# Kernel optimization log

Hardware: AMD Instinct MI355X
Metric: run time of the kernel (lower is better)

## Reference

```python
import jax, jax.numpy as jnp
import numpy as np

D_MODEL = 256
D_INNER = 512    # expand=2
D_STATE = 16
D_CONV = 4
DT_RANK = 16     # ceil(256/16)
N_BLOCKS = 4
EPS = 1e-5


def setup_inputs() -> dict:
    key = jax.random.key(0)
    ks = jax.random.split(key, 8)
    s = 0.02
    return {
        "x": jax.random.normal(ks[0], (1, 4, D_MODEL, 32, 32), jnp.float32),
        "norm_w": jnp.ones((N_BLOCKS, D_MODEL), jnp.float32),
        "norm_b": jnp.zeros((N_BLOCKS, D_MODEL), jnp.float32),
        "in_w": jax.random.normal(ks[1], (N_BLOCKS, 2 * D_INNER, D_MODEL), jnp.float32) * s,
        "conv_w": jax.random.normal(ks[2], (N_BLOCKS, D_INNER, D_CONV), jnp.float32) * s,
        "conv_b": jnp.zeros((N_BLOCKS, D_INNER), jnp.float32),
        "xproj_w": jax.random.normal(ks[3], (N_BLOCKS, DT_RANK + 2 * D_STATE, D_INNER), jnp.float32) * s,
        "dtproj_w": jax.random.normal(ks[4], (N_BLOCKS, D_INNER, DT_RANK), jnp.float32) * s,
        "dtproj_b": jax.random.normal(ks[5], (N_BLOCKS, D_INNER), jnp.float32) * s,
        "A_log": jnp.tile(jnp.log(jnp.arange(1, D_STATE + 1, dtype=jnp.float32))[None, None, :],
                          (N_BLOCKS, D_INNER, 1)),
        "Dp": jnp.ones((N_BLOCKS, D_INNER), jnp.float32),
        "out_w": jax.random.normal(ks[6], (N_BLOCKS, D_MODEL, D_INNER), jnp.float32) * s,
    }


def _layernorm(x, w, b):
    mu = jnp.mean(x, axis=-1, keepdims=True)
    var = jnp.var(x, axis=-1, keepdims=True)
    return (x - mu) / jnp.sqrt(var + EPS) * w + b


def _mamba(h, in_w, conv_w, conv_b, xproj_w, dtproj_w, dtproj_b, A_log, Dp, out_w):
    # h: (B, L, d_model)
    B, L, _ = h.shape
    xz = h @ in_w.T                                   # (B, L, 2*d_inner)
    x, z = jnp.split(xz, 2, axis=-1)
    # causal depthwise conv1d, kernel size D_CONV
    xp = jnp.pad(x, ((0, 0), (D_CONV - 1, 0), (0, 0)))
    xc = sum(xp[:, k:k + L, :] * conv_w[:, k] for k in range(D_CONV)) + conv_b
    x = jax.nn.silu(xc)                               # (B, L, d_inner)
    dbl = x @ xproj_w.T                               # (B, L, dt_rank + 2*d_state)
    dt = dbl[..., :DT_RANK]
    Bm = dbl[..., DT_RANK:DT_RANK + D_STATE]          # (B, L, n)
    Cm = dbl[..., DT_RANK + D_STATE:]                 # (B, L, n)
    dt = jax.nn.softplus(dt @ dtproj_w.T + dtproj_b)  # (B, L, d_inner)
    A = -jnp.exp(A_log)                               # (d_inner, n)
    dA = jnp.exp(dt[..., None] * A)                   # (B, L, d_inner, n)
    dBx = dt[..., None] * Bm[:, :, None, :] * x[..., None]

    def step(hprev, inp):
        dA_t, dBx_t, C_t = inp
        hcur = dA_t * hprev + dBx_t                   # (B, d_inner, n)
        return hcur, jnp.einsum('bdn,bn->bd', hcur, C_t)

    h0 = jnp.zeros((B, D_INNER, D_STATE), x.dtype)
    _, y = jax.lax.scan(step, h0, (dA.transpose(1, 0, 2, 3),
                                   dBx.transpose(1, 0, 2, 3),
                                   Cm.transpose(1, 0, 2)))
    y = y.transpose(1, 0, 2)                          # (B, L, d_inner)
    y = (y + Dp * x) * jax.nn.silu(z)
    return y @ out_w.T                                # (B, L, d_model)


def _forward(x, norm_w, norm_b, in_w, conv_w, conv_b, xproj_w, dtproj_w, dtproj_b, A_log, Dp, out_w):
    b, n, c, h, w = x.shape
    hs = x.reshape(b * n, c, h * w).transpose(0, 2, 1)  # (bn, hw, c)

    def blk(i, hidden, resid):
        resid = hidden if resid is None else resid + hidden
        hn = _layernorm(resid, norm_w[i], norm_b[i])
        out = _mamba(hn, in_w[i], conv_w[i], conv_b[i], xproj_w[i],
                     dtproj_w[i], dtproj_b[i], A_log[i], Dp[i], out_w[i])
        return out, resid

    res = None
    for i in range(2):  # pairs of (forward, backward-flipped) blocks
        hf, rf = blk(2 * i, hs, res)
        hb, rb = blk(2 * i + 1, hs[:, ::-1], None if res is None else res[:, ::-1])
        hs = hf + hb[:, ::-1]
        res = rf + rb[:, ::-1]
    res = res + hs
    return res.transpose(0, 2, 1).reshape(b, n, c, h, w)


def reference(x, norm_w, norm_b, in_w, conv_w, conv_b, xproj_w, dtproj_w, dtproj_b, A_log, Dp, out_w):
    return _forward(x, norm_w, norm_b, in_w, conv_w, conv_b, xproj_w,
                    dtproj_w, dtproj_b, A_log, Dp, out_w)
```

## Files before the change

kernel.cpp:

```cpp
#include <hip/hip_runtime.h>
#include <math.h>


__device__ __forceinline__ float sigmoidf_(float x){ return 1.f/(1.f+__expf(-x)); }
__device__ __forceinline__ short bf16_(float x){
  unsigned u = __float_as_uint(x);
  u += 0x7FFFu + ((u>>16)&1u);
  return (short)(u>>16);
}
__device__ __forceinline__ float f32_(short s){
  return __uint_as_float(((unsigned)(unsigned short)s)<<16);
}

using fragAB = __attribute__((ext_vector_type(8))) short;
using fragC  = __attribute__((ext_vector_type(4))) float;

__global__ __launch_bounds__(256) void k_transpose_in(const float* __restrict__ x, float* __restrict__ hs){
  __shared__ float tile[32][33];
  int b = blockIdx.z;
  int l0 = blockIdx.x*32, c0 = blockIdx.y*32;
  int tx = threadIdx.x, ty = threadIdx.y;
  #pragma unroll
  for (int j=0;j<32;j+=8)
    tile[ty+j][tx] = x[(size_t)b*262144 + (size_t)(c0+ty+j)*1024 + l0 + tx];
  __syncthreads();
  #pragma unroll
  for (int j=0;j<32;j+=8)
    hs[(size_t)b*262144 + (size_t)(l0+ty+j)*256 + (c0+tx)] = tile[tx][ty+j];
}

__global__ __launch_bounds__(256) void k_final(const float* __restrict__ racc, const float* __restrict__ hs, float* __restrict__ out){
  __shared__ float tile[32][33];
  int b = blockIdx.z;
  int l0 = blockIdx.x*32, c0 = blockIdx.y*32;
  int tx = threadIdx.x, ty = threadIdx.y;
  #pragma unroll
  for (int j=0;j<32;j+=8){
    size_t idx = (size_t)b*262144 + (size_t)(l0+ty+j)*256 + c0+tx;
    tile[ty+j][tx] = 2.f*racc[idx] + hs[idx];
  }
  __syncthreads();
  #pragma unroll
  for (int j=0;j<32;j+=8)
    out[(size_t)b*262144 + (size_t)(c0+ty+j)*1024 + l0+tx] = tile[tx][ty+j];
}

__global__ __launch_bounds__(256) void k_ln(const float* __restrict__ hs, float* __restrict__ racc, short* __restrict__ hn_f,
  const float* __restrict__ nw, const float* __restrict__ nb, int layer0, int first){
  int row = blockIdx.x, c = threadIdx.x;
  size_t idx = (size_t)row*256 + c;
  float r = hs[idx];
  if (!first) r += 2.f*racc[idx];
  racc[idx] = r;
  float s1=r, s2=r*r;
  #pragma unroll
  for (int o=32;o>=1;o>>=1){ s1+=__shfl_xor(s1,o); s2+=__shfl_xor(s2,o); }
  __shared__ float red[8];
  int wid=c>>6, lane=c&63;
  if (lane==0){ red[wid]=s1; red[4+wid]=s2; }
  __syncthreads();
  s1 = red[0]+red[1]+red[2]+red[3];
  s2 = red[4]+red[5]+red[6]+red[7];
  float mu = s1*(1.f/256.f);
  float var = s2*(1.f/256.f) - mu*mu;
  float inv = rsqrtf(var + 1e-5f);
  float nv = (r-mu)*inv;
  size_t fo = (((size_t)(row>>4)*32 + (c>>3))*16 + (row&15))*8 + (c&7);
  hn_f[fo]           = bf16_(nv*nw[layer0*256+c] + nb[layer0*256+c]);
  hn_f[1048576 + fo] = bf16_(nv*nw[(layer0+1)*256+c] + nb[(layer0+1)*256+c]);
}

__global__ __launch_bounds__(256) void k_wconv(
  const float* __restrict__ inw, const float* __restrict__ xpw,
  const float* __restrict__ dtw, const float* __restrict__ otw,
  short* __restrict__ f_inw, short* __restrict__ f_xpw,
  short* __restrict__ f_dtw, short* __restrict__ f_otw)
{
  int b = blockIdx.x, tid = threadIdx.x;
  int which, layer, idx;
  if (b < 4096){ which=0; layer=b>>10; idx=((b&1023)<<8)+tid; }
  else if (b < 4480){ int r=b-4096; which=1; layer=r/96;  idx=(r%96)*256+tid; }
  else if (b < 4736){ int r=b-4480; which=2; layer=r>>6;  idx=(r&63)*256+tid; }
  else              { int r=b-4736; which=3; layer=r>>9;  idx=(r&511)*256+tid; }
  const float* src; short* dst; int R,K,Kp;
  if (which==0){ src=inw; dst=f_inw; R=1024; K=256; Kp=256; }
  else if (which==1){ src=xpw; dst=f_xpw; R=48; K=512; Kp=512; }
  else if (which==2){ src=dtw; dst=f_dtw; R=512; K=16; Kp=32; }
  else { src=otw; dst=f_otw; R=256; K=512; Kp=512; }
  int per = (R>>4)*(Kp>>3)*128;
  int e = idx & 127, tile = idx >> 7;
  int nkt = Kp>>3;
  int kt = tile % nkt, rt = tile / nkt;
  int r = rt*16 + (e>>3), k = kt*8 + (e&7);
  float v = (k<K) ? src[((size_t)layer*R + r)*K + k] : 0.f;
  dst[(size_t)layer*per + idx] = bf16_(v);
}

__global__ __launch_bounds__(256) void k_mm4(
  const short* __restrict__ Af, long sA,
  const short* __restrict__ Wf, long sW,
  const short* __restrict__ A2f, const short* __restrict__ W2f,
  float* __restrict__ Cb, long sC,
  int K, int ldc, int mode,
  short* __restrict__ aux1, long sAux1,
  short* __restrict__ aux2, long sAux2)
{
  int z = blockIdx.z;
  int tid = threadIdx.x;
  int lane = tid & 63, wid = tid >> 6;
  int wm = wid & 1, wn = wid >> 1;
  int K8 = K >> 3;
  int mt_base = blockIdx.y*8 + wm*4;
  int nt_base = blockIdx.x*8 + wn*4;
  const int loff = lane*8;
  fragC acc[4][4] = {};
  const short* Aps[2] = { Af + (size_t)z*sA, A2f };
  const short* Wps[2] = { Wf + (size_t)z*sW, W2f };
  int nseg = A2f ? 2 : 1;
  for (int sgi=0; sgi<nseg; ++sgi){
    const short* A = Aps[sgi];
    const short* W = Wps[sgi];
    for (int kt=0; kt<K8; kt+=4){
      fragAB a[4], b[4];
      #pragma unroll
      for (int i=0;i<4;++i)
        a[i] = *(const fragAB*)(A + ((size_t)(mt_base+i)*K8 + kt)*128 + loff);
      #pragma unroll
      for (int j=0;j<4;++j)
        b[j] = *(const fragAB*)(W + ((size_t)(nt_base+j)*K8 + kt)*128 + loff);
      #pragma unroll
      for (int i=0;i<4;++i)
        #pragma unroll
        for (int j=0;j<4;++j)
          acc[i][j] = __builtin_amdgcn_mfma_f32_16x16x32_bf16(a[i], b[j], acc[i][j], 0,0,0);
    }
  }
  float* C = Cb ? Cb + (size_t)z*sC : nullptr;
  int r0 = (lane>>4)*4;
  int cc = lane & 15;
  #pragma unroll
  for (int i=0;i<4;++i){
    int row = (mt_base+i)*16 + r0;
    #pragma unroll
    for (int j=0;j<4;++j){
      int col = (nt_base+j)*16 + cc;
      #pragma unroll
      for (int r=0;r<4;++r){
        float v = acc[i][j][r];
        int rr = row + r;
        if (mode==3){
          if (col < 512) aux1[(size_t)z*sAux1 + (size_t)rr*512 + col] = bf16_(v);
          else           aux2[(size_t)z*sAux2 + (size_t)rr*512 + (col-512)] = bf16_(v);
        } else {
          C[(size_t)rr*ldc + col] = v;
        }
      }
    }
  }
}

__global__ __launch_bounds__(256) void k_xpdt(
  const short* __restrict__ xc_f, const short* __restrict__ wxp,
  const short* __restrict__ wdt, const float* __restrict__ dtb,
  float* __restrict__ dbl, float* __restrict__ dtv, int layer0)
{
  __shared__ short dt_lds[32][24];
  int z = blockIdx.y;
  int by = blockIdx.x;
  int layer = layer0 + z;
  int tid = threadIdx.x, lane = tid & 63, wn = tid >> 6;
  const short* A = xc_f + (size_t)z*2097152;
  const short* W = wxp + (size_t)layer*24576;
  int mt0 = by*2;
  const int loff = lane*8;
  int r0 = (lane>>4)*4, cc = lane & 15;
  {
    fragC acc[2] = {};
    int nt = wn < 3 ? wn : 2;
    for (int kt=0; kt<64; kt+=4){
      fragAB a0 = *(const fragAB*)(A + ((size_t)(mt0+0)*64 + kt)*128 + loff);
      fragAB a1 = *(const fragAB*)(A + ((size_t)(mt0+1)*64 + kt)*128 + loff);
      fragAB b  = *(const fragAB*)(W + ((size_t)nt*64 + kt)*128 + loff);
      acc[0] = __builtin_amdgcn_mfma_f32_16x16x32_bf16(a0, b, acc[0], 0,0,0);
      acc[1] = __builtin_amdgcn_mfma_f32_16x16x32_bf16(a1, b, acc[1], 0,0,0);
    }
    int col = nt*16 + cc;
    #pragma unroll
    for (int i=0;i<2;++i){
      int lr = i*16 + r0;
      int grow = by*32 + lr;
      #pragma unroll
      for (int r=0;r<4;++r){
        float v = acc[i][r];
        if (wn==1 || wn==2)
          dbl[(size_t)z*196608 + (size_t)(grow+r)*48 + col] = v;
        if (wn==0)
          dt_lds[lr+r][cc] = bf16_(v);
      }
    }
  }
  __syncthreads();
  {
    float* dto = dtv + (size_t)z*2097152;
    const float* bias = dtb + (size_t)layer*512;
    const short* WD = wdt + (size_t)layer*16384;
    int kq = lane >> 4;
    fragAB a2[2];
    #pragma unroll
    for (int i=0;i<2;++i){
      fragAB t = {};
      if (kq < 2){
        #pragma unroll
        for (int j=0;j<8;++j) t[j] = dt_lds[i*16 + (lane&15)][kq*8 + j];
      }
      a2[i] = t;
    }
    #pragma unroll
    for (int c2=0;c2<2;++c2){
      fragC acc2[2][4] = {};
      fragAB b2[4];
      #pragma unroll
      for (int j=0;j<4;++j){
        int ntj = wn*8 + c2*4 + j;
        b2[j] = *(const fragAB*)(WD + ((size_t)ntj*4)*128 + loff);
      }
      #pragma unroll
      for (int i=0;i<2;++i)
        #pragma unroll
        for (int j=0;j<4;++j)
          acc2[i][j] = __builtin_amdgcn_mfma_f32_16x16x32_bf16(a2[i], b2[j], acc2[i][j], 0,0,0);
      #pragma unroll
      for (int i=0;i<2;++i){
        int grow = by*32 + i*16 + r0;
        #pragma unroll
        for (int j=0;j<4;++j){
          int col2 = (wn*8 + c2*4 + j)*16 + cc;
          #pragma unroll
          for (int r=0;r<4;++r){
            float v = acc2[i][j][r] + bias[col2];
            v = (v > 20.f) ? v : log1pf(__expf(v));
            dto[(size_t)(grow+r)*512 + col2] = v;
          }
        }
      }
    }
  }
}

__global__ __launch_bounds__(256) void k_conv(const short* __restrict__ xb, short* __restrict__ xc_f,
  const float* __restrict__ cw, const float* __restrict__ cb, int layer0){
  int idx = blockIdx.x*256 + threadIdx.x;
  int d = idx & 511;
  int t = (idx >> 9) & 1023;
  int sb = idx >> 19;
  int s = sb >> 2, b = sb & 3;
  int layer = layer0 + s;
  const float* w = cw + ((size_t)layer*512 + d)*4;
  float accv = cb[(size_t)layer*512 + d];
  const short* xp = xb + (size_t)s*2097152 + (size_t)b*1024*512 + d;
  if (s==0){
    #pragma unroll
    for (int k=0;k<4;++k){ int tt = t + k - 3; if (tt>=0) accv = fmaf(f32_(xp[(size_t)tt*512]), w[k], accv); }
  } else {
    #pragma unroll
    for (int k=0;k<4;++k){ int tt = t + 3 - k; if (tt<1024) accv = fmaf(f32_(xp[(size_t)tt*512]), w[k], accv); }
  }
  float v = accv * sigmoidf_(accv);
  int row = b*1024 + t;
  xc_f[(size_t)s*2097152 + (((size_t)(row>>4)*64 + (d>>3))*16 + (row&15))*8 + (d&7)] = bf16_(v);
}

#define NCHUNK 64
#define CSTEPS 16

__device__ __forceinline__ float ld_xc(const short* xcf, int row, int d){
  return f32_(xcf[(((size_t)(row>>4)*64 + (d>>3))*16 + (row&15))*8 + (d&7)]);
}

__global__ __launch_bounds__(256) void k_scan_a(
  const float* __restrict__ dtv, const short* __restrict__ xc_f,
  const float* __restrict__ dbl, const float* __restrict__ A_log,
  float* __restrict__ dtsum, float* __restrict__ hF, int layer0)
{
  int d = blockIdx.x*256 + threadIdx.x;
  int k = blockIdx.y;
  int sb = blockIdx.z;
  int s = sb >> 2, b = sb & 3;
  int layer = layer0 + s;
  float Av[16];
  #pragma unroll
  for (int n=0;n<16;++n) Av[n] = -__expf(A_log[((size_t)layer*512 + d)*16 + n]);
  const float* dt_p = dtv + (size_t)sb*524288 + d;
  const short* xcf = xc_f + (size_t)s*2097152;
  const float* bc_p = dbl + (size_t)sb*49152;
  float h[16];
  #pragma unroll
  for (int n=0;n<16;++n) h[n] = 0.f;
  float ssum = 0.f;
  int u0 = k*CSTEPS;
  #pragma unroll
  for (int i=0;i<CSTEPS;++i){
    int u = u0 + i;
    int t = s ? (1023 - u) : u;
    int row = b*1024 + t;
    float dtval = dt_p[(size_t)t*512];
    float xv = ld_xc(xcf, row, d);
    const float4* bp = (const float4*)(bc_p + (size_t)t*48 + 16);
    float4 B0 = bp[0], B1 = bp[1], B2 = bp[2], B3 = bp[3];
    float Bv[16] = {B0.x,B0.y,B0.z,B0.w,B1.x,B1.y,B1.z,B1.w,
                    B2.x,B2.y,B2.z,B2.w,B3.x,B3.y,B3.z,B3.w};
    float w = dtval * xv;
    ssum += dtval;
    #pragma unroll
    for (int n=0;n<16;++n)
      h[n] = fmaf(__expf(dtval*Av[n]), h[n], w*Bv[n]);
  }
  size_t base = (size_t)(sb*NCHUNK + k)*512 + d;
  dtsum[base] = ssum;
  float4* hp = (float4*)(hF + base*16);
  #pragma unroll
  for (int q=0;q<4;++q) hp[q] = make_float4(h[4*q],h[4*q+1],h[4*q+2],h[4*q+3]);
}

__global__ __launch_bounds__(256) void k_scan_c(
  const float* __restrict__ dtsum, float* __restrict__ hF,
  const float* __restrict__ A_log, int layer0)
{
  __shared__ float tile[64][17];
  __shared__ float ds[64];
  int d = blockIdx.x, sb = blockIdx.y;
  int tid = threadIdx.x, lane = tid & 63, w = tid >> 6;
  int layer = layer0 + (sb >> 2);
  size_t base = (size_t)sb*64*8192 + (size_t)d*16;
  {
    int k = tid >> 2, n0 = (tid & 3)*4;
    float4 v = *(const float4*)(hF + base + (size_t)k*8192 + n0);
    tile[k][n0+0]=v.x; tile[k][n0+1]=v.y; tile[k][n0+2]=v.z; tile[k][n0+3]=v.w;
  }
  if (tid < 64) ds[tid] = dtsum[((size_t)sb*64 + tid)*512 + d];
  __syncthreads();
  float dsk = ds[lane];
  #pragma unroll
  for (int p=0;p<4;++p){
    int n = p*4 + w;
    float Av = -__expf(A_log[((size_t)layer*512 + d)*16 + n]);
    float a = __expf(Av * dsk);
    float h = tile[lane][n];
    #pragma unroll
    for (int o=1;o<64;o<<=1){
      float au = __shfl_up(a, o);
      float hu = __shfl_up(h, o);
      if (lane >= o){ h = fmaf(a, hu, h); a *= au; }
    }
    float h0 = __shfl_up(h, 1);
    if (lane == 0) h0 = 0.f;
    tile[lane][n] = h0;
  }
  __syncthreads();
  {
    int k = tid >> 2, n0 = (tid & 3)*4;
    float4 v = make_float4(tile[k][n0], tile[k][n0+1], tile[k][n0+2], tile[k][n0+3]);
    *(float4*)(hF + base + (size_t)k*8192 + n0) = v;
  }
}

__global__ __launch_bounds__(256) void k_scan_b(
  const float* __restrict__ dtv, const short* __restrict__ xc_f, const short* __restrict__ zb,
  const float* __restrict__ dbl, const float* __restrict__ A_log, const float* __restrict__ Dp,
  const float* __restrict__ h0p, short* __restrict__ y_f, int layer0)
{
  int d = blockIdx.x*256 + threadIdx.x;
  int k = blockIdx.y;
  int sb = blockIdx.z;
  int s = sb >> 2, b = sb & 3;
  int layer = layer0 + s;
  float Av[16];
  #pragma unroll
  for (int n=0;n<16;++n) Av[n] = -__expf(A_log[((size_t)layer*512 + d)*16 + n]);
  float Dv = Dp[(size_t)layer*512 + d];
  const float* dt_p = dtv + (size_t)sb*524288 + d;
  const short* xcf = xc_f + (size_t)s*2097152;
  const short* z_p = zb + (size_t)s*2097152 + (size_t)b*1024*512 + d;
  const float* bc_p = dbl + (size_t)sb*49152;
  size_t base = (size_t)(sb*NCHUNK + k)*512 + d;
  float h[16];
  const float4* hp = (const float4*)(h0p + base*16);
  #pragma unroll
  for (int q=0;q<4;++q){
    float4 v = hp[q];
    h[4*q]=v.x; h[4*q+1]=v.y; h[4*q+2]=v.z; h[4*q+3]=v.w;
  }
  short* yo = y_f + (size_t)s*2097152;
  int u0 = k*CSTEPS;
  #pragma unroll
  for (int i=0;i<CSTEPS;++i){
    int u = u0 + i;
    int t = s ? (1023 - u) : u;
    int row = b*1024 + t;
    float dtval = dt_p[(size_t)t*512];
    float xv = ld_xc(xcf, row, d);
    const float4* bp = (const float4*)(bc_p + (size_t)t*48 + 16);
    float4 B0 = bp[0], B1 = bp[1], B2 = bp[2], B3 = bp[3];
    float4 C0 = bp[4], C1 = bp[5], C2 = bp[6], C3 = bp[7];
    float Bv[16] = {B0.x,B0.y,B0.z,B0.w,B1.x,B1.y,B1.z,B1.w,
                    B2.x,B2.y,B2.z,B2.w,B3.x,B3.y,B3.z,B3.w};
    float Cv[16] = {C0.x,C0.y,C0.z,C0.w,C1.x,C1.y,C1.z,C1.w,
                    C2.x,C2.y,C2.z,C2.w,C3.x,C3.y,C3.z,C3.w};
    float w = dtval * xv;
    float y = 0.f;
    #pragma unroll
    for (int n=0;n<16;++n){
      h[n] = fmaf(__expf(dtval*Av[n]), h[n], w*Bv[n]);
      y = fmaf(h[n], Cv[n], y);
    }
    float zv = f32_(z_p[(size_t)t*512]);
    float yv = (y + Dv*xv) * (zv*sigmoidf_(zv));
    yo[(((size_t)(row>>4)*64 + (d>>3))*16 + (row&15))*8 + (d&7)] = bf16_(yv);
  }
}

extern "C" void kernel_launch(void* const* d_in, const int* in_sizes, int n_in,
                              void* d_out, int out_size, void* d_ws, size_t ws_size,
                              hipStream_t stream) {
  const float* x        = (const float*)d_in[0];
  const float* norm_w   = (const float*)d_in[1];
  const float* norm_b   = (const float*)d_in[2];
  const float* in_w     = (const float*)d_in[3];
  const float* conv_w   = (const float*)d_in[4];
  const float* conv_b   = (const float*)d_in[5];
  const float* xproj_w  = (const float*)d_in[6];
  const float* dtproj_w = (const float*)d_in[7];
  const float* dtproj_b = (const float*)d_in[8];
  const float* A_log    = (const float*)d_in[9];
  const float* Dp       = (const float*)d_in[10];
  const float* out_w    = (const float*)d_in[11];
  float* out = (float*)d_out;
  float* ws = (float*)d_ws;

  float* hs    = ws;
  float* racc  = ws + 1048576;
  short* hn_f  = (short*)(ws + 2097152);
  short* xb    = (short*)(ws + 3145728);
  short* zb    = (short*)(ws + 5242880);
  short* xc_f  = (short*)(ws + 7340032);
  short* y_f   = (short*)(ws + 9437184);
  float* dbl   = ws + 11534336;
  float* dtv   = ws + 12058624;
  float* dtsum = ws + 16252928;
  float* hF    = ws + 16515072;
  short* w_inw = (short*)(ws + 20709376);
  short* w_xp  = w_inw + 1048576;
  short* w_dt  = w_xp + 98304;
  short* w_out = w_dt + 65536;

  k_wconv<<<6784, 256, 0, stream>>>(in_w, xproj_w, dtproj_w, out_w, w_inw, w_xp, w_dt, w_out);
  k_transpose_in<<<dim3(32,8,4), dim3(32,8), 0, stream>>>(x, hs);

  for (int it=0; it<2; ++it){
    int layer0 = 2*it;
    k_ln<<<4096, 256, 0, stream>>>(hs, racc, hn_f, norm_w, norm_b, layer0, it==0 ? 1 : 0);
    k_mm4<<<dim3(8,32,2), 256, 0, stream>>>(hn_f, 1048576L, w_inw + (size_t)layer0*262144, 262144L,
        nullptr, nullptr, nullptr, 0L, 256, 0, 3, xb, 2097152L, zb, 2097152L);
    k_conv<<<16384, 256, 0, stream>>>(xb, xc_f, conv_w, conv_b, layer0);
    k_xpdt<<<dim3(128,2), 256, 0, stream>>>(xc_f, w_xp, w_dt, dtproj_b, dbl, dtv, layer0);
    k_scan_a<<<dim3(2,NCHUNK,8), 256, 0, stream>>>(dtv, xc_f, dbl, A_log, dtsum, hF, layer0);
    k_scan_c<<<dim3(512,8), 256, 0, stream>>>(dtsum, hF, A_log, layer0);
    k_scan_b<<<dim3(2,NCHUNK,8), 256, 0, stream>>>(dtv, xc_f, zb, dbl, A_log, Dp, hF, y_f, layer0);
    k_mm4<<<dim3(2,32,1), 256, 0, stream>>>(y_f, 0L, w_out + (size_t)layer0*131072, 0L,
        y_f + 2097152, w_out + (size_t)(layer0+1)*131072, hs, 0L, 512, 256, 0,
        nullptr, 0L, nullptr, 0L);
  }
  k_final<<<dim3(32,8,4), dim3(32,8), 0, stream>>>(racc, hs, out);
}
```

Before: 446.3 us.

## Fuse layernorm into in-proj GMM and causal conv into x-proj kernel

Layernorm is now computed inside the in-projection matmul kernel: normalized rows are built as bf16 in LDS, which removes the separate LN kernel and its global round trip. Each of the 8 column blocks recomputes the LN for its rows. The depthwise causal conv plus SiLU moves into the x-proj kernel and feeds the MFMA from LDS while still writing xc_f for the scans. The out-projection gets a dedicated kernel with smaller 64x64 tiles, giving 256 blocks instead of 64 for better occupancy. Residual accumulation is double-buffered (raccA/raccB) so blocks that read and write it concurrently do not race.

```diff
diff --git a/kernel.cpp b/kernel.cpp
--- a/kernel.cpp
+++ b/kernel.cpp
@@ -1,6 +1,9 @@
 #include <hip/hip_runtime.h>
 #include <math.h>
 
+
+#define NCHUNK 64
+#define CSTEPS 16
 
 __device__ __forceinline__ float sigmoidf_(float x){ return 1.f/(1.f+__expf(-x)); }
 __device__ __forceinline__ short bf16_(float x){
@@ -43,31 +46,6 @@
   #pragma unroll
   for (int j=0;j<32;j+=8)
     out[(size_t)b*262144 + (size_t)(c0+ty+j)*1024 + l0+tx] = tile[tx][ty+j];
-}
-
-__global__ __launch_bounds__(256) void k_ln(const float* __restrict__ hs, float* __restrict__ racc, short* __restrict__ hn_f,
-  const float* __restrict__ nw, const float* __restrict__ nb, int layer0, int first){
-  int row = blockIdx.x, c = threadIdx.x;
-  size_t idx = (size_t)row*256 + c;
-  float r = hs[idx];
-  if (!first) r += 2.f*racc[idx];
-  racc[idx] = r;
-  float s1=r, s2=r*r;
-  #pragma unroll
-  for (int o=32;o>=1;o>>=1){ s1+=__shfl_xor(s1,o); s2+=__shfl_xor(s2,o); }
-  __shared__ float red[8];
-  int wid=c>>6, lane=c&63;
-  if (lane==0){ red[wid]=s1; red[4+wid]=s2; }
-  __syncthreads();
-  s1 = red[0]+red[1]+red[2]+red[3];
-  s2 = red[4]+red[5]+red[6]+red[7];
-  float mu = s1*(1.f/256.f);
-  float var = s2*(1.f/256.f) - mu*mu;
-  float inv = rsqrtf(var + 1e-5f);
-  float nv = (r-mu)*inv;
-  size_t fo = (((size_t)(row>>4)*32 + (c>>3))*16 + (row&15))*8 + (c&7);
-  hn_f[fo]           = bf16_(nv*nw[layer0*256+c] + nb[layer0*256+c]);
-  hn_f[1048576 + fo] = bf16_(nv*nw[(layer0+1)*256+c] + nb[(layer0+1)*256+c]);
 }
 
 __global__ __launch_bounds__(256) void k_wconv(
@@ -96,51 +74,67 @@
   dst[(size_t)layer*per + idx] = bf16_(v);
 }
 
-__global__ __launch_bounds__(256) void k_mm4(
-  const short* __restrict__ Af, long sA,
-  const short* __restrict__ Wf, long sW,
-  const short* __restrict__ A2f, const short* __restrict__ W2f,
-  float* __restrict__ Cb, long sC,
-  int K, int ldc, int mode,
-  short* __restrict__ aux1, long sAux1,
-  short* __restrict__ aux2, long sAux2)
-{
-  int z = blockIdx.z;
-  int tid = threadIdx.x;
-  int lane = tid & 63, wid = tid >> 6;
-  int wm = wid & 1, wn = wid >> 1;
-  int K8 = K >> 3;
-  int mt_base = blockIdx.y*8 + wm*4;
-  int nt_base = blockIdx.x*8 + wn*4;
+__global__ __launch_bounds__(256) void k_fmm(
+  const float* __restrict__ hs, const float* __restrict__ racc_in, float* __restrict__ racc_out,
+  const float* __restrict__ nw, const float* __restrict__ nb,
+  const short* __restrict__ w_in_base, short* __restrict__ xb, short* __restrict__ zb,
+  int layer0, int first)
+{
+  __shared__ short As[32768];
+  int s = blockIdx.z, bx = blockIdx.x, my = blockIdx.y;
+  int layer = layer0 + s;
+  int tid = threadIdx.x, lane = tid & 63, w = tid >> 6;
+  int m0 = my*128;
+  int c0 = lane*4;
+  for (int i=0;i<32;++i){
+    int lr = w*32 + i;
+    size_t idx = (size_t)(m0+lr)*256 + c0;
+    float4 rv = *(const float4*)(hs + idx);
+    if (!first){
+      float4 ra = *(const float4*)(racc_in + idx);
+      rv.x += 2.f*ra.x; rv.y += 2.f*ra.y; rv.z += 2.f*ra.z; rv.w += 2.f*ra.w;
+    }
+    if (bx==0 && s==0) *(float4*)(racc_out + idx) = rv;
+    float s1 = rv.x+rv.y+rv.z+rv.w;
+    float s2 = rv.x*rv.x+rv.y*rv.y+rv.z*rv.z+rv.w*rv.w;
+    #pragma unroll
+    for (int o=32;o>=1;o>>=1){ s1+=__shfl_xor(s1,o); s2+=__shfl_xor(s2,o); }
+    float mu = s1*(1.f/256.f);
+    float var = s2*(1.f/256.f) - mu*mu;
+    float inv = rsqrtf(var+1e-5f);
+    float4 g = *(const float4*)(nw + (size_t)layer*256 + c0);
+    float4 be = *(const float4*)(nb + (size_t)layer*256 + c0);
+    int la = ((lr>>4)*32 + (c0>>3))*128 + (lr&15)*8 + (c0&7);
+    As[la+0] = bf16_((rv.x-mu)*inv*g.x + be.x);
+    As[la+1] = bf16_((rv.y-mu)*inv*g.y + be.y);
+    As[la+2] = bf16_((rv.z-mu)*inv*g.z + be.z);
+    As[la+3] = bf16_((rv.w-mu)*inv*g.w + be.w);
+  }
+  __syncthreads();
+  int wm = w & 1, wn = w >> 1;
+  int mt_base = wm*4;
+  int nt_base = bx*8 + wn*4;
+  const short* W = w_in_base + (size_t)layer*262144;
   const int loff = lane*8;
   fragC acc[4][4] = {};
-  const short* Aps[2] = { Af + (size_t)z*sA, A2f };
-  const short* Wps[2] = { Wf + (size_t)z*sW, W2f };
-  int nseg = A2f ? 2 : 1;
-  for (int sgi=0; sgi<nseg; ++sgi){
-    const short* A = Aps[sgi];
-    const short* W = Wps[sgi];
-    for (int kt=0; kt<K8; kt+=4){
-      fragAB a[4], b[4];
-      #pragma unroll
-      for (int i=0;i<4;++i)
-        a[i] = *(const fragAB*)(A + ((size_t)(mt_base+i)*K8 + kt)*128 + loff);
+  for (int kt=0; kt<32; kt+=4){
+    fragAB a[4], bfr[4];
+    #pragma unroll
+    for (int i=0;i<4;++i)
+      a[i] = *(const fragAB*)(As + ((mt_base+i)*32 + kt)*128 + loff);
+    #pragma unroll
+    for (int j=0;j<4;++j)
+      bfr[j] = *(const fragAB*)(W + ((size_t)(nt_base+j)*32 + kt)*128 + loff);
+    #pragma unroll
+    for (int i=0;i<4;++i)
       #pragma unroll
       for (int j=0;j<4;++j)
-        b[j] = *(const fragAB*)(W + ((size_t)(nt_base+j)*K8 + kt)*128 + loff);
-      #pragma unroll
-      for (int i=0;i<4;++i)
-        #pragma unroll
-        for (int j=0;j<4;++j)
-          acc[i][j] = __builtin_amdgcn_mfma_f32_16x16x32_bf16(a[i], b[j], acc[i][j], 0,0,0);
-    }
-  }
-  float* C = Cb ? Cb + (size_t)z*sC : nullptr;
-  int r0 = (lane>>4)*4;
-  int cc = lane & 15;
+        acc[i][j] = __builtin_amdgcn_mfma_f32_16x16x32_bf16(a[i], bfr[j], acc[i][j], 0,0,0);
+  }
+  int r0 = (lane>>4)*4, cc = lane & 15;
   #pragma unroll
   for (int i=0;i<4;++i){
-    int row = (mt_base+i)*16 + r0;
+    int row = m0 + (mt_base+i)*16 + r0;
     #pragma unroll
     for (int j=0;j<4;++j){
       int col = (nt_base+j)*16 + cc;
@@ -148,41 +142,75 @@
       for (int r=0;r<4;++r){
         float v = acc[i][j][r];
         int rr = row + r;
-        if (mode==3){
-          if (col < 512) aux1[(size_t)z*sAux1 + (size_t)rr*512 + col] = bf16_(v);
-          else           aux2[(size_t)z*sAux2 + (size_t)rr*512 + (col-512)] = bf16_(v);
-        } else {
-          C[(size_t)rr*ldc + col] = v;
-        }
+        if (col < 512) xb[(size_t)s*2097152 + (size_t)rr*512 + col] = bf16_(v);
+        else           zb[(size_t)s*2097152 + (size_t)rr*512 + (col-512)] = bf16_(v);
       }
     }
   }
 }
 
 __global__ __launch_bounds__(256) void k_xpdt(
-  const short* __restrict__ xc_f, const short* __restrict__ wxp,
-  const short* __restrict__ wdt, const float* __restrict__ dtb,
+  const short* __restrict__ xb, short* __restrict__ xc_f,
+  const float* __restrict__ cw, const float* __restrict__ cb,
+  const short* __restrict__ wxp, const short* __restrict__ wdt, const float* __restrict__ dtb,
   float* __restrict__ dbl, float* __restrict__ dtv, int layer0)
 {
+  __shared__ short xcs[16384];
   __shared__ short dt_lds[32][24];
-  int z = blockIdx.y;
-  int by = blockIdx.x;
+  int z = blockIdx.y, by = blockIdx.x;
   int layer = layer0 + z;
   int tid = threadIdx.x, lane = tid & 63, wn = tid >> 6;
-  const short* A = xc_f + (size_t)z*2097152;
-  const short* W = wxp + (size_t)layer*24576;
-  int mt0 = by*2;
+  int b = by >> 5, l0 = (by & 31) << 5;
+  {
+    int d0 = tid*2;
+    const short* xs = xb + (size_t)z*2097152 + (size_t)b*524288;
+    float wt[2][4], bias2[2];
+    #pragma unroll
+    for (int q=0;q<2;++q){
+      float4 wv = *(const float4*)(cw + ((size_t)layer*512 + d0 + q)*4);
+      wt[q][0]=wv.x; wt[q][1]=wv.y; wt[q][2]=wv.z; wt[q][3]=wv.w;
+      bias2[q] = cb[(size_t)layer*512 + d0 + q];
+    }
+    float xm[3][2];
+    short* xg = xc_f + (size_t)z*2097152;
+    #pragma unroll
+    for (int q=0;q<3;++q){
+      int l = z==0 ? (l0-3+q) : (l0+34-q);
+      if (l<0 || l>1023){ xm[q][0]=0.f; xm[q][1]=0.f; }
+      else { unsigned u = *(const unsigned*)(xs + (size_t)l*512 + d0);
+             xm[q][0]=f32_((short)(u&0xFFFF)); xm[q][1]=f32_((short)(u>>16)); }
+    }
+    for (int step=0; step<32; ++step){
+      int i = z==0 ? step : (31-step);
+      int l = l0 + i;
+      unsigned u = *(const unsigned*)(xs + (size_t)l*512 + d0);
+      float xt0 = f32_((short)(u&0xFFFF)), xt1 = f32_((short)(u>>16));
+      float a0 = bias2[0] + wt[0][0]*xm[0][0] + wt[0][1]*xm[1][0] + wt[0][2]*xm[2][0] + wt[0][3]*xt0;
+      float a1 = bias2[1] + wt[1][0]*xm[0][1] + wt[1][1]*xm[1][1] + wt[1][2]*xm[2][1] + wt[1][3]*xt1;
+      float v0 = a0*sigmoidf_(a0), v1 = a1*sigmoidf_(a1);
+      unsigned pv = (unsigned)(unsigned short)bf16_(v0) | ((unsigned)(unsigned short)bf16_(v1)<<16);
+      int la = ((i>>4)*64 + (d0>>3))*128 + (i&15)*8 + (d0&7);
+      *(unsigned*)(xcs + la) = pv;
+      int grow = b*1024 + l;
+      *(unsigned*)(xg + (((size_t)(grow>>4)*64 + (size_t)(d0>>3))*128 + (size_t)(grow&15)*8 + (d0&7))) = pv;
+      xm[0][0]=xm[1][0]; xm[0][1]=xm[1][1];
+      xm[1][0]=xm[2][0]; xm[1][1]=xm[2][1];
+      xm[2][0]=xt0;      xm[2][1]=xt1;
+    }
+  }
+  __syncthreads();
   const int loff = lane*8;
   int r0 = (lane>>4)*4, cc = lane & 15;
   {
     fragC acc[2] = {};
     int nt = wn < 3 ? wn : 2;
+    const short* Wx = wxp + (size_t)layer*24576;
     for (int kt=0; kt<64; kt+=4){
-      fragAB a0 = *(const fragAB*)(A + ((size_t)(mt0+0)*64 + kt)*128 + loff);
-      fragAB a1 = *(const fragAB*)(A + ((size_t)(mt0+1)*64 + kt)*128 + loff);
-      fragAB b  = *(const fragAB*)(W + ((size_t)nt*64 + kt)*128 + loff);
-      acc[0] = __builtin_amdgcn_mfma_f32_16x16x32_bf16(a0, b, acc[0], 0,0,0);
-      acc[1] = __builtin_amdgcn_mfma_f32_16x16x32_bf16(a1, b, acc[1], 0,0,0);
+      fragAB a0 = *(const fragAB*)(xcs + (0*64 + kt)*128 + loff);
+      fragAB a1 = *(const fragAB*)(xcs + (1*64 + kt)*128 + loff);
+      fragAB bb = *(const fragAB*)(Wx + ((size_t)nt*64 + kt)*128 + loff);
+      acc[0] = __builtin_amdgcn_mfma_f32_16x16x32_bf16(a0, bb, acc[0], 0,0,0);
+      acc[1] = __builtin_amdgcn_mfma_f32_16x16x32_bf16(a1, bb, acc[1], 0,0,0);
     }
     int col = nt*16 + cc;
     #pragma unroll
@@ -247,32 +275,6 @@
   }
 }
 
-__global__ __launch_bounds__(256) void k_conv(const short* __restrict__ xb, short* __restrict__ xc_f,
-  const float* __restrict__ cw, const float* __restrict__ cb, int layer0){
-  int idx = blockIdx.x*256 + threadIdx.x;
-  int d = idx & 511;
-  int t = (idx >> 9) & 1023;
-  int sb = idx >> 19;
-  int s = sb >> 2, b = sb & 3;
-  int layer = layer0 + s;
-  const float* w = cw + ((size_t)layer*512 + d)*4;
-  float accv = cb[(size_t)layer*512 + d];
-  const short* xp = xb + (size_t)s*2097152 + (size_t)b*1024*512 + d;
-  if (s==0){
-    #pragma unroll
-    for (int k=0;k<4;++k){ int tt = t + k - 3; if (tt>=0) accv = fmaf(f32_(xp[(size_t)tt*512]), w[k], accv); }
-  } else {
-    #pragma unroll
-    for (int k=0;k<4;++k){ int tt = t + 3 - k; if (tt<1024) accv = fmaf(f32_(xp[(size_t)tt*512]), w[k], accv); }
-  }
-  float v = accv * sigmoidf_(accv);
-  int row = b*1024 + t;
-  xc_f[(size_t)s*2097152 + (((size_t)(row>>4)*64 + (d>>3))*16 + (row&15))*8 + (d&7)] = bf16_(v);
-}
-
-#define NCHUNK 64
-#define CSTEPS 16
-
 __device__ __forceinline__ float ld_xc(const short* xcf, int row, int d){
   return f32_(xcf[(((size_t)(row>>4)*64 + (d>>3))*16 + (row&15))*8 + (d&7)]);
 }
@@ -380,7 +382,7 @@
   float Dv = Dp[(size_t)layer*512 + d];
   const float* dt_p = dtv + (size_t)sb*524288 + d;
   const short* xcf = xc_f + (size_t)s*2097152;
-  const short* z_p = zb + (size_t)s*2097152 + (size_t)b*1024*512 + d;
+  const short* z_p = zb + (size_t)s*2097152 + (size_t)b*524288 + d;
   const float* bc_p = dbl + (size_t)sb*49152;
   size_t base = (size_t)(sb*NCHUNK + k)*512 + d;
   float h[16];
@@ -416,6 +418,53 @@
     float zv = f32_(z_p[(size_t)t*512]);
     float yv = (y + Dv*xv) * (zv*sigmoidf_(zv));
     yo[(((size_t)(row>>4)*64 + (d>>3))*16 + (row&15))*8 + (d&7)] = bf16_(yv);
+  }
+}
+
+__global__ __launch_bounds__(256) void k_mmo(
+  const short* __restrict__ Af, const short* __restrict__ Wf,
+  const short* __restrict__ A2f, const short* __restrict__ W2f,
+  float* __restrict__ C)
+{
+  int tid = threadIdx.x;
+  int lane = tid & 63, wid = tid >> 6;
+  int wm = wid & 1, wn = wid >> 1;
+  int mt_base = blockIdx.y*4 + wm*2;
+  int nt_base = blockIdx.x*4 + wn*2;
+  const int K8 = 64;
+  const int loff = lane*8;
+  fragC acc[2][2] = {};
+  const short* Aps[2] = { Af, A2f };
+  const short* Wps[2] = { Wf, W2f };
+  for (int sgi=0; sgi<2; ++sgi){
+    const short* A = Aps[sgi];
+    const short* W = Wps[sgi];
+    for (int kt=0; kt<K8; kt+=4){
+      fragAB a[2], bfr[2];
+      #pragma unroll
+      for (int i=0;i<2;++i)
+        a[i] = *(const fragAB*)(A + ((size_t)(mt_base+i)*K8 + kt)*128 + loff);
+      #pragma unroll
+      for (int j=0;j<2;++j)
+        bfr[j] = *(const fragAB*)(W + ((size_t)(nt_base+j)*K8 + kt)*128 + loff);
+      #pragma unroll
+      for (int i=0;i<2;++i)
+        #pragma unroll
+        for (int j=0;j<2;++j)
+          acc[i][j] = __builtin_amdgcn_mfma_f32_16x16x32_bf16(a[i], bfr[j], acc[i][j], 0,0,0);
+    }
+  }
+  int r0 = (lane>>4)*4, cc = lane & 15;
+  #pragma unroll
+  for (int i=0;i<2;++i){
+    int row = (mt_base+i)*16 + r0;
+    #pragma unroll
+    for (int j=0;j<2;++j){
+      int col = (nt_base+j)*16 + cc;
+      #pragma unroll
+      for (int r=0;r<4;++r)
+        C[(size_t)(row+r)*256 + col] = acc[i][j][r];
+    }
   }
 }
 
@@ -438,17 +487,17 @@
   float* ws = (float*)d_ws;
 
   float* hs    = ws;
-  float* racc  = ws + 1048576;
-  short* hn_f  = (short*)(ws + 2097152);
+  float* raccA = ws + 1048576;
+  float* raccB = ws + 2097152;
   short* xb    = (short*)(ws + 3145728);
   short* zb    = (short*)(ws + 5242880);
   short* xc_f  = (short*)(ws + 7340032);
   short* y_f   = (short*)(ws + 9437184);
   float* dbl   = ws + 11534336;
-  float* dtv   = ws + 12058624;
-  float* dtsum = ws + 16252928;
-  float* hF    = ws + 16515072;
-  short* w_inw = (short*)(ws + 20709376);
+  float* dtv   = ws + 11927552;
+  float* dtsum = ws + 16121856;
+  float* hF    = ws + 16384000;
+  short* w_inw = (short*)(ws + 20578304);
   short* w_xp  = w_inw + 1048576;
   short* w_dt  = w_xp + 98304;
   short* w_out = w_dt + 65536;
@@ -458,17 +507,15 @@
 
   for (int it=0; it<2; ++it){
     int layer0 = 2*it;
-    k_ln<<<4096, 256, 0, stream>>>(hs, racc, hn_f, norm_w, norm_b, layer0, it==0 ? 1 : 0);
-    k_mm4<<<dim3(8,32,2), 256, 0, stream>>>(hn_f, 1048576L, w_inw + (size_t)layer0*262144, 262144L,
-        nullptr, nullptr, nullptr, 0L, 256, 0, 3, xb, 2097152L, zb, 2097152L);
-    k_conv<<<16384, 256, 0, stream>>>(xb, xc_f, conv_w, conv_b, layer0);
-    k_xpdt<<<dim3(128,2), 256, 0, stream>>>(xc_f, w_xp, w_dt, dtproj_b, dbl, dtv, layer0);
+    k_fmm<<<dim3(8,32,2), 256, 0, stream>>>(hs, it ? raccA : nullptr, it ? raccB : raccA,
+        norm_w, norm_b, w_inw, xb, zb, layer0, it==0 ? 1 : 0);
+    k_xpdt<<<dim3(128,2), 256, 0, stream>>>(xb, xc_f, conv_w, conv_b,
+        w_xp, w_dt, dtproj_b, dbl, dtv, layer0);
     k_scan_a<<<dim3(2,NCHUNK,8), 256, 0, stream>>>(dtv, xc_f, dbl, A_log, dtsum, hF, layer0);
     k_scan_c<<<dim3(512,8), 256, 0, stream>>>(dtsum, hF, A_log, layer0);
     k_scan_b<<<dim3(2,NCHUNK,8), 256, 0, stream>>>(dtv, xc_f, zb, dbl, A_log, Dp, hF, y_f, layer0);
-    k_mm4<<<dim3(2,32,1), 256, 0, stream>>>(y_f, 0L, w_out + (size_t)layer0*131072, 0L,
-        y_f + 2097152, w_out + (size_t)(layer0+1)*131072, hs, 0L, 512, 256, 0,
-        nullptr, 0L, nullptr, 0L);
-  }
-  k_final<<<dim3(32,8,4), dim3(32,8), 0, stream>>>(racc, hs, out);
-}
+    k_mmo<<<dim3(4,64), 256, 0, stream>>>(y_f, w_out + (size_t)layer0*131072,
+        y_f + 2097152, w_out + (size_t)(layer0+1)*131072, hs);
+  }
+  k_final<<<dim3(32,8,4), dim3(32,8), 0, stream>>>(raccB, hs, out);
+}
```

Result: faster. 384.5 us (-13.8%).
